# Kernel optimization log

Measured on AMD Instinct MI355X. Metric: run time of the kernel, lower is better.

## Reference

```python
import jax, jax.numpy as jnp
import numpy as np
import math

B, S, DIM = 2, 2048, 1024
H, KVH = 16, 4
HD = DIM // H          # 64, head dim
WINDOW = 256           # sliding-window size (0 = global)
ROPE_BASE = 10000.0
EPS = 1e-6


def setup_inputs() -> dict:
    key = jax.random.key(0)
    ks = jax.random.split(key, 6)
    s = 0.02
    return {
        "x": jax.random.normal(ks[0], (B, S, DIM), jnp.float32),
        "Wq": jax.random.normal(ks[1], (DIM, DIM), jnp.float32) * s,
        "Wk": jax.random.normal(ks[2], (KVH * HD, DIM), jnp.float32) * s,
        "Wv": jax.random.normal(ks[3], (KVH * HD, DIM), jnp.float32) * s,
        "Wo": jax.random.normal(ks[4], (DIM, DIM), jnp.float32) * s,
        "q_gain": jnp.ones((H,), jnp.float32),
        "pair_mix": jnp.tile(jnp.eye(2, dtype=jnp.float32), (H // 2, 1, 1))
                    + 0.01 * jax.random.normal(ks[5], (H // 2, 2, 2), jnp.float32),
    }


def _rms_norm(v):
    # F.rms_norm over last dim, no learned weight
    return v * jax.lax.rsqrt(jnp.mean(v * v, axis=-1, keepdims=True) + EPS)


def _rope_tables(seqlen, dtype):
    inv_freq = 1.0 / (ROPE_BASE ** (jnp.arange(0, HD, 2, dtype=jnp.float32) / HD))  # [HD/2]
    t = jnp.arange(seqlen, dtype=jnp.float32)
    freqs = jnp.outer(t, inv_freq)                        # [S, HD/2]
    return jnp.cos(freqs).astype(dtype)[None, None], jnp.sin(freqs).astype(dtype)[None, None]


def _apply_rotary(v, cos, sin):
    half = v.shape[-1] // 2
    v1, v2 = v[..., :half], v[..., half:]
    return jnp.concatenate((v1 * cos + v2 * sin, -v1 * sin + v2 * cos), axis=-1)


def reference(x, Wq, Wk, Wv, Wo, q_gain, pair_mix):
    bsz, seqlen, dim = x.shape
    q = (x @ Wq.T).reshape(bsz, seqlen, H, HD).transpose(0, 2, 1, 3)    # [B,H,S,D]
    k = (x @ Wk.T).reshape(bsz, seqlen, KVH, HD).transpose(0, 2, 1, 3)  # [B,KV,S,D]
    v = (x @ Wv.T).reshape(bsz, seqlen, KVH, HD).transpose(0, 2, 1, 3)

    q = _rms_norm(q)
    k = _rms_norm(k)
    cos, sin = _rope_tables(seqlen, q.dtype)
    q = _apply_rotary(q, cos, sin)
    k = _apply_rotary(k, cos, sin)
    q = q * q_gain.astype(q.dtype)[None, :, None, None]

    # GQA expansion (repeat_interleave over head axis)
    rep = H // KVH
    k_full = jnp.repeat(k, rep, axis=1)  # [B,H,S,D]
    v_full = jnp.repeat(v, rep, axis=1)

    # sliding-window causal mask: attend iff 0 <= i-j < WINDOW
    pos = jnp.arange(seqlen)
    mask = (pos[:, None] >= pos[None, :]) & (pos[:, None] - pos[None, :] < WINDOW)

    scale = 1.0 / math.sqrt(HD)
    scores = jnp.einsum('bhqd,bhkd->bhqk', q, k_full) * scale
    scores = jnp.where(mask[None, None], scores, jnp.finfo(scores.dtype).min)
    att = jax.nn.softmax(scores, axis=-1)
    y = jnp.einsum('bhqk,bhkd->bhqd', att, v_full)  # [B,H,S,D]

    # paired-head mixing: mix each consecutive head pair with a 2x2 matrix
    yp = y.reshape(bsz, H // 2, 2, seqlen, HD)
    y = jnp.einsum('bpitd,poi->bpotd', yp, pair_mix.astype(y.dtype)).reshape(bsz, H, seqlen, HD)

    out = y.transpose(0, 2, 1, 3).reshape(bsz, seqlen, dim) @ Wo.T
    return out
```

## Files before the change

### kernel.cpp

```cpp
#include <hip/hip_runtime.h>
#include <hip/hip_bf16.h>
#include <cstdint>

#define S_LEN 2048
#define QKV_COLS 1536

typedef __bf16 bf16_t;
typedef bf16_t bf16x8 __attribute__((ext_vector_type(8)));
typedef bf16_t bf16x4 __attribute__((ext_vector_type(4)));
typedef float f32x4 __attribute__((ext_vector_type(4)));

typedef __attribute__((address_space(1))) void as1_void;
typedef __attribute__((address_space(3))) void as3_void;

__device__ __forceinline__ void async_load16(const void* g, void* lds) {
  __builtin_amdgcn_global_load_lds(
      (as1_void*)(uintptr_t)g,
      (as3_void*)(uint32_t)(uintptr_t)lds,
      16, 0, 0);
}

__global__ __launch_bounds__(256) void convert_all(
    const float4* __restrict__ x, const float4* __restrict__ wq,
    const float4* __restrict__ wk, const float4* __restrict__ wv,
    const float4* __restrict__ wo, const float* __restrict__ pm,
    bf16x4* __restrict__ xb, bf16x4* __restrict__ wqkvb, bf16x4* __restrict__ wob) {
  int u = blockIdx.x * 256 + threadIdx.x;
  if (u >= 1441792) {
    int off = u - 1441792;
    int flat = off * 4;
    int row = flat >> 10, colf = flat & 1023;
    int col2p = colf & ~64;
    int p = colf >> 7, ii = (colf >> 6) & 1;
    float4 a = wo[(row * 1024 + col2p) >> 2];
    float4 bq = wo[(row * 1024 + (col2p | 64)) >> 2];
    float m0v = pm[p * 4 + ii], m1v = pm[p * 4 + 2 + ii];
    bf16x4 o4;
    o4[0] = (bf16_t)(m0v * a.x + m1v * bq.x);
    o4[1] = (bf16_t)(m0v * a.y + m1v * bq.y);
    o4[2] = (bf16_t)(m0v * a.z + m1v * bq.z);
    o4[3] = (bf16_t)(m0v * a.w + m1v * bq.w);
    wob[off] = o4;
    return;
  }
  const float4* src; bf16x4* dst; int off;
  if (u < 1048576)      { src = x;  dst = xb;             off = u; }
  else if (u < 1310720) { src = wq; dst = wqkvb;          off = u - 1048576; }
  else if (u < 1376256) { src = wk; dst = wqkvb + 262144; off = u - 1310720; }
  else                  { src = wv; dst = wqkvb + 327680; off = u - 1376256; }
  float4 f = src[off];
  bf16x4 o;
  o[0] = (bf16_t)f.x; o[1] = (bf16_t)f.y; o[2] = (bf16_t)f.z; o[3] = (bf16_t)f.w;
  dst[off] = o;
}

__global__ __launch_bounds__(256) void gemm_qkv(
    const bf16_t* __restrict__ A, const bf16_t* __restrict__ B,
    bf16_t* __restrict__ C, bf16_t* __restrict__ vt,
    const float* __restrict__ q_gain, int N, int K) {
  __shared__ bf16_t As[128 * 64];
  __shared__ bf16_t Bs[128 * 64];
  const int tid = threadIdx.x;
  const int lane = tid & 63;
  const int w = tid >> 6;
  const int wm = (w & 1) << 6, wn = (w >> 1) << 6;
  const int orig = blockIdx.y * gridDim.x + blockIdx.x;
  const int id = (orig & 7) * 48 + (orig >> 3);
  const int m0 = (id / 12) << 7, n0 = (id % 12) << 7;
  const int fidx = lane & 15, quad = lane >> 4;
  f32x4 acc[4][4] = {};
  const bf16_t* Ag[4];
  const bf16_t* Bg[4];
#pragma unroll
  for (int j = 0; j < 4; j++) {
    int c = tid + j * 256, r = c >> 3, s = (c & 7) ^ (r & 7);
    Ag[j] = A + (size_t)(m0 + r) * K + s * 8;
    Bg[j] = B + (size_t)(n0 + r) * K + s * 8;
  }
  int aoff[4][2], boff[4][2];
#pragma unroll
  for (int i = 0; i < 4; i++) {
    int arow = wm + i * 16 + fidx;
    int brow = wn + i * 16 + fidx;
#pragma unroll
    for (int half = 0; half < 2; half++) {
      aoff[i][half] = arow * 64 + (((half * 4 + quad) ^ (arow & 7)) * 8);
      boff[i][half] = brow * 64 + (((half * 4 + quad) ^ (brow & 7)) * 8);
    }
  }
  for (int kt = 0; kt < K; kt += 64) {
    __syncthreads();
#pragma unroll
    for (int j = 0; j < 4; j++) {
      async_load16(Ag[j] + kt, As + (tid + j * 256) * 8);
      async_load16(Bg[j] + kt, Bs + (tid + j * 256) * 8);
    }
    __syncthreads();
    bf16x8 af[4][2], bfr[4][2];
#pragma unroll
    for (int i = 0; i < 4; i++)
#pragma unroll
      for (int half = 0; half < 2; half++) {
        af[i][half]  = *(const bf16x8*)(As + aoff[i][half]);
        bfr[i][half] = *(const bf16x8*)(Bs + boff[i][half]);
      }
#pragma unroll
    for (int half = 0; half < 2; half++)
#pragma unroll
      for (int mi = 0; mi < 4; mi++)
#pragma unroll
        for (int ni = 0; ni < 4; ni++)
          acc[mi][ni] = __builtin_amdgcn_mfma_f32_16x16x32_bf16(
              af[mi][half], bfr[ni][half], acc[mi][ni], 0, 0, 0);
  }
  const int hc0 = n0 + wn;
  if (hc0 >= 1280) {
#pragma unroll
    for (int mi = 0; mi < 4; mi++)
#pragma unroll
      for (int ni = 0; ni < 4; ni++) {
        int cg = (hc0 - 1280) + ni * 16 + fidx;
        int g = cg >> 6, dh = cg & 63;
        int srow = m0 + wm + mi * 16 + quad * 4;
        int bb = srow >> 11, si = srow & (S_LEN - 1);
        bf16x4 pack;
#pragma unroll
        for (int r = 0; r < 4; r++) pack[r] = (bf16_t)acc[mi][ni][r];
        *(bf16x4*)(vt + ((size_t)((bb * 4 + g) * 64 + dh)) * S_LEN + si) = pack;
      }
    return;
  }
  float gain = 1.f;
  if (hc0 < 1024) gain = q_gain[hc0 >> 6] * 0.125f;
#pragma unroll
  for (int mi = 0; mi < 4; mi++)
#pragma unroll
    for (int r = 0; r < 4; r++) {
      float ss = 0.f;
#pragma unroll
      for (int ni = 0; ni < 4; ni++) { float t = acc[mi][ni][r]; ss += t * t; }
#pragma unroll
      for (int off = 8; off >= 1; off >>= 1) ss += __shfl_xor(ss, off);
      float scl = rsqrtf(ss * (1.f / 64.f) + 1e-6f);
      int s = (m0 + wm + mi * 16 + quad * 4 + r) & (S_LEN - 1);
#pragma unroll
      for (int ni = 0; ni < 2; ni++) {
        float v1 = acc[mi][ni][r] * scl;
        float v2 = acc[mi][ni + 2][r] * scl;
        float fr = (float)(ni * 16 + fidx);
        float ang = (float)s * __expf(fr * -0.28782313662425575f);
        float sn, cs;
        __sincosf(ang, &sn, &cs);
        acc[mi][ni][r]     = (v1 * cs + v2 * sn) * gain;
        acc[mi][ni + 2][r] = (-v1 * sn + v2 * cs) * gain;
      }
    }
#pragma unroll
  for (int mi = 0; mi < 4; mi++)
#pragma unroll
    for (int ni = 0; ni < 4; ni++)
#pragma unroll
      for (int r = 0; r < 4; r++) {
        int gr = m0 + wm + mi * 16 + quad * 4 + r;
        int gc = n0 + wn + ni * 16 + fidx;
        C[(size_t)gr * N + gc] = (bf16_t)acc[mi][ni][r];
      }
}

__global__ __launch_bounds__(256) void gemm_bt_f32(
    const bf16_t* __restrict__ A, const bf16_t* __restrict__ B,
    float* __restrict__ C, int N, int K) {
  __shared__ bf16_t As[128 * 64];
  __shared__ bf16_t Bs[128 * 64];
  const int tid = threadIdx.x;
  const int lane = tid & 63;
  const int w = tid >> 6;
  const int wm = (w & 1) << 6, wn = (w >> 1) << 6;
  const int orig = blockIdx.y * gridDim.x + blockIdx.x;
  const int id = (orig & 7) * 32 + (orig >> 3);
  const int m0 = (id >> 3) << 7, n0 = (id & 7) << 7;
  const int fidx = lane & 15, quad = lane >> 4;
  f32x4 acc[4][4] = {};
  const bf16_t* Ag[4];
  const bf16_t* Bg[4];
#pragma unroll
  for (int j = 0; j < 4; j++) {
    int c = tid + j * 256, r = c >> 3, s = (c & 7) ^ (r & 7);
    Ag[j] = A + (size_t)(m0 + r) * K + s * 8;
    Bg[j] = B + (size_t)(n0 + r) * K + s * 8;
  }
  int aoff[4][2], boff[4][2];
#pragma unroll
  for (int i = 0; i < 4; i++) {
    int arow = wm + i * 16 + fidx;
    int brow = wn + i * 16 + fidx;
#pragma unroll
    for (int half = 0; half < 2; half++) {
      aoff[i][half] = arow * 64 + (((half * 4 + quad) ^ (arow & 7)) * 8);
      boff[i][half] = brow * 64 + (((half * 4 + quad) ^ (brow & 7)) * 8);
    }
  }
  for (int kt = 0; kt < K; kt += 64) {
    __syncthreads();
#pragma unroll
    for (int j = 0; j < 4; j++) {
      async_load16(Ag[j] + kt, As + (tid + j * 256) * 8);
      async_load16(Bg[j] + kt, Bs + (tid + j * 256) * 8);
    }
    __syncthreads();
    bf16x8 af[4][2], bfr[4][2];
#pragma unroll
    for (int i = 0; i < 4; i++)
#pragma unroll
      for (int half = 0; half < 2; half++) {
        af[i][half]  = *(const bf16x8*)(As + aoff[i][half]);
        bfr[i][half] = *(const bf16x8*)(Bs + boff[i][half]);
      }
#pragma unroll
    for (int half = 0; half < 2; half++)
#pragma unroll
      for (int mi = 0; mi < 4; mi++)
#pragma unroll
        for (int ni = 0; ni < 4; ni++)
          acc[mi][ni] = __builtin_amdgcn_mfma_f32_16x16x32_bf16(
              af[mi][half], bfr[ni][half], acc[mi][ni], 0, 0, 0);
  }
#pragma unroll
  for (int mi = 0; mi < 4; mi++)
#pragma unroll
    for (int ni = 0; ni < 4; ni++)
#pragma unroll
      for (int r = 0; r < 4; r++) {
        int gr = m0 + wm + mi * 16 + quad * 4 + r;
        int gc = n0 + wn + ni * 16 + fidx;
        C[(size_t)gr * N + gc] = acc[mi][ni][r];
      }
}

#define FIXMAX 8.0f
#define PST 40
#define OST 72
__global__ __launch_bounds__(256) void attn_mfma(
    const bf16_t* __restrict__ qkv, const bf16_t* __restrict__ vt,
    bf16_t* __restrict__ yb) {
  __shared__ bf16_t plds[4][16 * PST];
  __shared__ bf16_t ob[4][32 * OST];
  const int tid = threadIdx.x, lane = tid & 63, w = tid >> 6;
  const int col = lane & 15, quad = lane >> 4;
  const int orig = blockIdx.z * 256 + blockIdx.y * 64 + blockIdx.x;
  const int id = (orig & 7) * 64 + (orig >> 3);
  const int q0 = (id & 63) * 32, g = (id >> 6) & 3, b = id >> 8;
  const int h = g * 4 + w;

  bf16x8 qf[2][2];
#pragma unroll
  for (int t = 0; t < 2; t++) {
    const bf16_t* qb =
        qkv + ((size_t)b * S_LEN + q0 + t * 16 + col) * QKV_COLS + h * 64 + quad * 8;
    qf[t][0] = *(const bf16x8*)qb;
    qf[t][1] = *(const bf16x8*)(qb + 32);
  }
  const bf16_t* kbase = qkv + (size_t)b * S_LEN * QKV_COLS + 1024 + g * 64 + quad * 8;
  const bf16_t* vbase = vt + ((size_t)((b * 4 + g) * 64) + col) * S_LEN + quad * 8;

  f32x4 o[2][4] = {};
  float ps[2][4] = {};

  const int c_lo = max(0, (q0 - 255) >> 5);
  const int c_hi = (q0 + 31) >> 5;
  for (int c = c_lo; c <= c_hi; c++) {
    const int k0 = c * 32;
    bf16x8 kf[2][2];
#pragma unroll
    for (int nt = 0; nt < 2; nt++) {
      const bf16_t* kp = kbase + (size_t)(k0 + nt * 16 + col) * QKV_COLS;
      kf[nt][0] = *(const bf16x8*)kp;
      kf[nt][1] = *(const bf16x8*)(kp + 32);
    }
    bf16x8 vf[4];
#pragma unroll
    for (int nt2 = 0; nt2 < 4; nt2++)
      vf[nt2] = *(const bf16x8*)(vbase + (size_t)(nt2 * 16) * S_LEN + k0);

#pragma unroll
    for (int t = 0; t < 2; t++) {
      const int qt0 = q0 + t * 16;
      if (k0 > qt0 + 15) continue;
      f32x4 s[2];
#pragma unroll
      for (int nt = 0; nt < 2; nt++) {
        f32x4 a = {};
        a = __builtin_amdgcn_mfma_f32_16x16x32_bf16(qf[t][0], kf[nt][0], a, 0, 0, 0);
        a = __builtin_amdgcn_mfma_f32_16x16x32_bf16(qf[t][1], kf[nt][1], a, 0, 0, 0);
        s[nt] = a;
      }
      const bool needmask = (k0 + 31 > qt0) || (k0 < qt0 - 224);
      if (needmask) {
#pragma unroll
        for (int r = 0; r < 4; r++) {
          int q = qt0 + quad * 4 + r;
#pragma unroll
          for (int nt = 0; nt < 2; nt++) {
            int k = k0 + nt * 16 + col;
            bool valid = (k <= q) && (q - k < 256);
            float p = valid ? __expf(s[nt][r] - FIXMAX) : 0.f;
            ps[t][r] += p;
            plds[w][(quad * 4 + r) * PST + nt * 16 + col] = (bf16_t)p;
          }
        }
      } else {
#pragma unroll
        for (int r = 0; r < 4; r++) {
#pragma unroll
          for (int nt = 0; nt < 2; nt++) {
            float p = __expf(s[nt][r] - FIXMAX);
            ps[t][r] += p;
            plds[w][(quad * 4 + r) * PST + nt * 16 + col] = (bf16_t)p;
          }
        }
      }
      asm volatile("s_waitcnt lgkmcnt(0)" ::: "memory");
      bf16x8 pf = *(const bf16x8*)(plds[w] + col * PST + quad * 8);
#pragma unroll
      for (int nt2 = 0; nt2 < 4; nt2++)
        o[t][nt2] = __builtin_amdgcn_mfma_f32_16x16x32_bf16(pf, vf[nt2], o[t][nt2], 0, 0, 0);
    }
  }
#pragma unroll
  for (int t = 0; t < 2; t++)
#pragma unroll
    for (int r = 0; r < 4; r++) {
      float v = ps[t][r];
#pragma unroll
      for (int off = 8; off >= 1; off >>= 1) v += __shfl_xor(v, off);
      float il = 1.f / v;
      int row = t * 16 + quad * 4 + r;
#pragma unroll
      for (int nt2 = 0; nt2 < 4; nt2++)
        ob[w][row * OST + nt2 * 16 + col] = (bf16_t)(o[t][nt2][r] * il);
    }
  asm volatile("s_waitcnt lgkmcnt(0)" ::: "memory");
#pragma unroll
  for (int it = 0; it < 4; it++) {
    int row = it * 8 + (lane >> 3);
    int d0 = (lane & 7) * 8;
    bf16x8 v8 = *(const bf16x8*)(ob[w] + row * OST + d0);
    *(bf16x8*)(yb + ((size_t)b * S_LEN + q0 + row) * 1024 + h * 64 + d0) = v8;
  }
}

extern "C" void kernel_launch(void* const* d_in, const int* in_sizes, int n_in,
                              void* d_out, int out_size, void* d_ws, size_t ws_size,
                              hipStream_t stream) {
  const float* x        = (const float*)d_in[0];
  const float* Wq       = (const float*)d_in[1];
  const float* Wk       = (const float*)d_in[2];
  const float* Wv       = (const float*)d_in[3];
  const float* Wo       = (const float*)d_in[4];
  const float* q_gain   = (const float*)d_in[5];
  const float* pair_mix = (const float*)d_in[6];
  float* out = (float*)d_out;

  bf16_t* ws    = (bf16_t*)d_ws;
  bf16_t* xb    = ws;
  bf16_t* wqkvb = xb + 4096 * 1024;
  bf16_t* wob   = wqkvb + 1536 * 1024;
  bf16_t* qkvb  = wob + 1024 * 1024;
  bf16_t* yb    = qkvb + 4096 * 1536;
  bf16_t* vt    = yb + 4096 * 1024;

  convert_all<<<6656, 256, 0, stream>>>(
      (const float4*)x, (const float4*)Wq, (const float4*)Wk, (const float4*)Wv,
      (const float4*)Wo, pair_mix, (bf16x4*)xb, (bf16x4*)wqkvb, (bf16x4*)wob);
  gemm_qkv<<<dim3(12, 32), 256, 0, stream>>>(xb, wqkvb, qkvb, vt, q_gain, 1536, 1024);
  attn_mfma<<<dim3(64, 4, 2), 256, 0, stream>>>(qkvb, vt, yb);
  gemm_bt_f32<<<dim3(8, 32), 256, 0, stream>>>(yb, wob, out, 1024, 1024);
}
```

Baseline: 153.0 us.

## Double-buffer GEMM LDS tiles and keep attention probabilities in registers

Both GEMM kernels now use two LDS buffers per operand and prefetch the next K-tile with async global-to-LDS loads while MFMAs run on the current tile. This replaces the two full syncthreads per iteration with a vmcnt wait and barriers, overlapping load latency with compute at the cost of doubled LDS use and lower occupancy. In attention, the QK^T MFMA operands are swapped so each lane holds scores for one query column. The probability tile is then packed to bf16 and redistributed with cross-lane shuffles instead of a round trip through LDS, and the row-sum reduction is simplified to match.

```diff
diff --git a/kernel.cpp b/kernel.cpp
--- a/kernel.cpp
+++ b/kernel.cpp
@@ -18,6 +18,12 @@
       (as1_void*)(uintptr_t)g,
       (as3_void*)(uint32_t)(uintptr_t)lds,
       16, 0, 0);
+}
+
+__device__ __forceinline__ uint32_t pkbf(float a, float b) {
+  union { bf16_t h[2]; uint32_t u; } c;
+  c.h[0] = (bf16_t)a; c.h[1] = (bf16_t)b;
+  return c.u;
 }
 
 __global__ __launch_bounds__(256) void convert_all(
@@ -58,8 +64,8 @@
     const bf16_t* __restrict__ A, const bf16_t* __restrict__ B,
     bf16_t* __restrict__ C, bf16_t* __restrict__ vt,
     const float* __restrict__ q_gain, int N, int K) {
-  __shared__ bf16_t As[128 * 64];
-  __shared__ bf16_t Bs[128 * 64];
+  __shared__ bf16_t As[2][128 * 64];
+  __shared__ bf16_t Bs[2][128 * 64];
   const int tid = threadIdx.x;
   const int lane = tid & 63;
   const int w = tid >> 6;
@@ -88,21 +94,33 @@
       boff[i][half] = brow * 64 + (((half * 4 + quad) ^ (brow & 7)) * 8);
     }
   }
+#pragma unroll
+  for (int j = 0; j < 4; j++) {
+    async_load16(Ag[j], &As[0][(tid + j * 256) * 8]);
+    async_load16(Bg[j], &Bs[0][(tid + j * 256) * 8]);
+  }
+  int cur = 0;
   for (int kt = 0; kt < K; kt += 64) {
-    __syncthreads();
-#pragma unroll
-    for (int j = 0; j < 4; j++) {
-      async_load16(Ag[j] + kt, As + (tid + j * 256) * 8);
-      async_load16(Bg[j] + kt, Bs + (tid + j * 256) * 8);
-    }
-    __syncthreads();
+    const int nk = kt + 64;
+    if (nk < K) {
+#pragma unroll
+      for (int j = 0; j < 4; j++) {
+        async_load16(Ag[j] + nk, &As[cur ^ 1][(tid + j * 256) * 8]);
+        async_load16(Bg[j] + nk, &Bs[cur ^ 1][(tid + j * 256) * 8]);
+      }
+      asm volatile("s_waitcnt vmcnt(8)" ::: "memory");
+    } else {
+      asm volatile("s_waitcnt vmcnt(0)" ::: "memory");
+    }
+    __builtin_amdgcn_s_barrier();
+    __builtin_amdgcn_sched_barrier(0);
     bf16x8 af[4][2], bfr[4][2];
 #pragma unroll
     for (int i = 0; i < 4; i++)
 #pragma unroll
       for (int half = 0; half < 2; half++) {
-        af[i][half]  = *(const bf16x8*)(As + aoff[i][half]);
-        bfr[i][half] = *(const bf16x8*)(Bs + boff[i][half]);
+        af[i][half]  = *(const bf16x8*)(&As[cur][aoff[i][half]]);
+        bfr[i][half] = *(const bf16x8*)(&Bs[cur][boff[i][half]]);
       }
 #pragma unroll
     for (int half = 0; half < 2; half++)
@@ -112,6 +130,9 @@
         for (int ni = 0; ni < 4; ni++)
           acc[mi][ni] = __builtin_amdgcn_mfma_f32_16x16x32_bf16(
               af[mi][half], bfr[ni][half], acc[mi][ni], 0, 0, 0);
+    asm volatile("s_waitcnt lgkmcnt(0)" ::: "memory");
+    __builtin_amdgcn_s_barrier();
+    cur ^= 1;
   }
   const int hc0 = n0 + wn;
   if (hc0 >= 1280) {
@@ -170,8 +191,8 @@
 __global__ __launch_bounds__(256) void gemm_bt_f32(
     const bf16_t* __restrict__ A, const bf16_t* __restrict__ B,
     float* __restrict__ C, int N, int K) {
-  __shared__ bf16_t As[128 * 64];
-  __shared__ bf16_t Bs[128 * 64];
+  __shared__ bf16_t As[2][128 * 64];
+  __shared__ bf16_t Bs[2][128 * 64];
   const int tid = threadIdx.x;
   const int lane = tid & 63;
   const int w = tid >> 6;
@@ -200,21 +221,33 @@
       boff[i][half] = brow * 64 + (((half * 4 + quad) ^ (brow & 7)) * 8);
     }
   }
+#pragma unroll
+  for (int j = 0; j < 4; j++) {
+    async_load16(Ag[j], &As[0][(tid + j * 256) * 8]);
+    async_load16(Bg[j], &Bs[0][(tid + j * 256) * 8]);
+  }
+  int cur = 0;
   for (int kt = 0; kt < K; kt += 64) {
-    __syncthreads();
-#pragma unroll
-    for (int j = 0; j < 4; j++) {
-      async_load16(Ag[j] + kt, As + (tid + j * 256) * 8);
-      async_load16(Bg[j] + kt, Bs + (tid + j * 256) * 8);
-    }
-    __syncthreads();
+    const int nk = kt + 64;
+    if (nk < K) {
+#pragma unroll
+      for (int j = 0; j < 4; j++) {
+        async_load16(Ag[j] + nk, &As[cur ^ 1][(tid + j * 256) * 8]);
+        async_load16(Bg[j] + nk, &Bs[cur ^ 1][(tid + j * 256) * 8]);
+      }
+      asm volatile("s_waitcnt vmcnt(8)" ::: "memory");
+    } else {
+      asm volatile("s_waitcnt vmcnt(0)" ::: "memory");
+    }
+    __builtin_amdgcn_s_barrier();
+    __builtin_amdgcn_sched_barrier(0);
     bf16x8 af[4][2], bfr[4][2];
 #pragma unroll
     for (int i = 0; i < 4; i++)
 #pragma unroll
       for (int half = 0; half < 2; half++) {
-        af[i][half]  = *(const bf16x8*)(As + aoff[i][half]);
-        bfr[i][half] = *(const bf16x8*)(Bs + boff[i][half]);
+        af[i][half]  = *(const bf16x8*)(&As[cur][aoff[i][half]]);
+        bfr[i][half] = *(const bf16x8*)(&Bs[cur][boff[i][half]]);
       }
 #pragma unroll
     for (int half = 0; half < 2; half++)
@@ -224,6 +257,9 @@
         for (int ni = 0; ni < 4; ni++)
           acc[mi][ni] = __builtin_amdgcn_mfma_f32_16x16x32_bf16(
               af[mi][half], bfr[ni][half], acc[mi][ni], 0, 0, 0);
+    asm volatile("s_waitcnt lgkmcnt(0)" ::: "memory");
+    __builtin_amdgcn_s_barrier();
+    cur ^= 1;
   }
 #pragma unroll
   for (int mi = 0; mi < 4; mi++)
@@ -238,12 +274,10 @@
 }
 
 #define FIXMAX 8.0f
-#define PST 40
 #define OST 72
 __global__ __launch_bounds__(256) void attn_mfma(
     const bf16_t* __restrict__ qkv, const bf16_t* __restrict__ vt,
     bf16_t* __restrict__ yb) {
-  __shared__ bf16_t plds[4][16 * PST];
   __shared__ bf16_t ob[4][32 * OST];
   const int tid = threadIdx.x, lane = tid & 63, w = tid >> 6;
   const int col = lane & 15, quad = lane >> 4;
@@ -264,7 +298,7 @@
   const bf16_t* vbase = vt + ((size_t)((b * 4 + g) * 64) + col) * S_LEN + quad * 8;
 
   f32x4 o[2][4] = {};
-  float ps[2][4] = {};
+  float ps[2] = {};
 
   const int c_lo = max(0, (q0 - 255) >> 5);
   const int c_hi = (q0 + 31) >> 5;
@@ -286,59 +320,72 @@
     for (int t = 0; t < 2; t++) {
       const int qt0 = q0 + t * 16;
       if (k0 > qt0 + 15) continue;
-      f32x4 s[2];
+      f32x4 st[2];
 #pragma unroll
       for (int nt = 0; nt < 2; nt++) {
         f32x4 a = {};
-        a = __builtin_amdgcn_mfma_f32_16x16x32_bf16(qf[t][0], kf[nt][0], a, 0, 0, 0);
-        a = __builtin_amdgcn_mfma_f32_16x16x32_bf16(qf[t][1], kf[nt][1], a, 0, 0, 0);
-        s[nt] = a;
+        a = __builtin_amdgcn_mfma_f32_16x16x32_bf16(kf[nt][0], qf[t][0], a, 0, 0, 0);
+        a = __builtin_amdgcn_mfma_f32_16x16x32_bf16(kf[nt][1], qf[t][1], a, 0, 0, 0);
+        st[nt] = a;
       }
       const bool needmask = (k0 + 31 > qt0) || (k0 < qt0 - 224);
+      float p2[2][4];
       if (needmask) {
-#pragma unroll
-        for (int r = 0; r < 4; r++) {
-          int q = qt0 + quad * 4 + r;
-#pragma unroll
-          for (int nt = 0; nt < 2; nt++) {
-            int k = k0 + nt * 16 + col;
+        int q = qt0 + col;
+#pragma unroll
+        for (int nt = 0; nt < 2; nt++)
+#pragma unroll
+          for (int r = 0; r < 4; r++) {
+            int k = k0 + nt * 16 + quad * 4 + r;
             bool valid = (k <= q) && (q - k < 256);
-            float p = valid ? __expf(s[nt][r] - FIXMAX) : 0.f;
-            ps[t][r] += p;
-            plds[w][(quad * 4 + r) * PST + nt * 16 + col] = (bf16_t)p;
+            p2[nt][r] = valid ? __expf(st[nt][r] - FIXMAX) : 0.f;
           }
-        }
       } else {
 #pragma unroll
-        for (int r = 0; r < 4; r++) {
-#pragma unroll
-          for (int nt = 0; nt < 2; nt++) {
-            float p = __expf(s[nt][r] - FIXMAX);
-            ps[t][r] += p;
-            plds[w][(quad * 4 + r) * PST + nt * 16 + col] = (bf16_t)p;
-          }
-        }
-      }
-      asm volatile("s_waitcnt lgkmcnt(0)" ::: "memory");
-      bf16x8 pf = *(const bf16x8*)(plds[w] + col * PST + quad * 8);
+        for (int nt = 0; nt < 2; nt++)
+#pragma unroll
+          for (int r = 0; r < 4; r++)
+            p2[nt][r] = __expf(st[nt][r] - FIXMAX);
+      }
+#pragma unroll
+      for (int nt = 0; nt < 2; nt++)
+#pragma unroll
+        for (int r = 0; r < 4; r++) ps[t] += p2[nt][r];
+      uint32_t pk0[2], pk1[2];
+      pk0[0] = pkbf(p2[0][0], p2[0][1]); pk0[1] = pkbf(p2[0][2], p2[0][3]);
+      pk1[0] = pkbf(p2[1][0], p2[1][1]); pk1[1] = pkbf(p2[1][2], p2[1][3]);
+      uint32_t w32[4];
+#pragma unroll
+      for (int m = 0; m < 4; m++) {
+        int srclane = col + 16 * ((2 * quad + (m >> 1)) & 3);
+        uint32_t a0 = (uint32_t)__shfl((int)pk0[m & 1], srclane);
+        uint32_t a1 = (uint32_t)__shfl((int)pk1[m & 1], srclane);
+        w32[m] = (quad < 2) ? a0 : a1;
+      }
+      union { uint32_t u[4]; bf16x8 v; } pu;
+      pu.u[0] = w32[0]; pu.u[1] = w32[1]; pu.u[2] = w32[2]; pu.u[3] = w32[3];
+      bf16x8 pf = pu.v;
 #pragma unroll
       for (int nt2 = 0; nt2 < 4; nt2++)
         o[t][nt2] = __builtin_amdgcn_mfma_f32_16x16x32_bf16(pf, vf[nt2], o[t][nt2], 0, 0, 0);
     }
   }
 #pragma unroll
-  for (int t = 0; t < 2; t++)
-#pragma unroll
-    for (int r = 0; r < 4; r++) {
-      float v = ps[t][r];
-#pragma unroll
-      for (int off = 8; off >= 1; off >>= 1) v += __shfl_xor(v, off);
-      float il = 1.f / v;
-      int row = t * 16 + quad * 4 + r;
-#pragma unroll
-      for (int nt2 = 0; nt2 < 4; nt2++)
-        ob[w][row * OST + nt2 * 16 + col] = (bf16_t)(o[t][nt2][r] * il);
-    }
+  for (int t = 0; t < 2; t++) {
+    float v = ps[t];
+    v += __shfl_xor(v, 16);
+    v += __shfl_xor(v, 32);
+    float il = 1.f / v;
+    float il4[4];
+#pragma unroll
+    for (int r = 0; r < 4; r++) il4[r] = __shfl(il, quad * 4 + r);
+    int row0 = t * 16 + quad * 4;
+#pragma unroll
+    for (int nt2 = 0; nt2 < 4; nt2++)
+#pragma unroll
+      for (int r = 0; r < 4; r++)
+        ob[w][(row0 + r) * OST + nt2 * 16 + col] = (bf16_t)(o[t][nt2][r] * il4[r]);
+  }
   asm volatile("s_waitcnt lgkmcnt(0)" ::: "memory");
 #pragma unroll
   for (int it = 0; it < 4; it++) {
```

New measurement: 140.5 us. 8.2% less time.
